# Kernel tuning notes

Hardware: AMD Instinct MI355X
Metric: run time of the kernel (lower is better)

The kernel has to match this reference:

```python
import jax, jax.numpy as jnp
import numpy as np

H = 2048          # hidden_size
NH = 16           # num query heads
NKV = 8           # num kv heads
HD = 128          # head_dim
T = 4096          # tokens (single causal prefill sequence)
THETA = 1000000.0
EPS = 1e-6
QS = NH * HD
KVS = NKV * HD
SCALE = HD ** -0.5


def setup_inputs() -> dict:
    key = jax.random.key(0)
    k0, k1, k2 = jax.random.split(key, 3)
    return {
        "positions": jnp.arange(T, dtype=jnp.int32),
        "hidden_states": jax.random.normal(k0, (T, H), jnp.float32),
        "w_qkv": jax.random.normal(k1, (H, QS + 2 * KVS), jnp.float32) * 0.02,
        "w_o": jax.random.normal(k2, (QS, H), jnp.float32) * 0.02,
        "q_norm_w": jnp.ones((HD,), jnp.float32),
        "k_norm_w": jnp.ones((HD,), jnp.float32),
    }


def _rmsnorm(x, w):
    # per-head RMSNorm over last dim (head_dim)
    return x * jax.lax.rsqrt(jnp.mean(x * x, axis=-1, keepdims=True) + EPS) * w


def _rope(x, cos, sin):
    # neox-style rotate-half RoPE; x: [T, nheads, HD], cos/sin: [T, 1, HD/2]
    x1, x2 = jnp.split(x, 2, axis=-1)
    return jnp.concatenate([x1 * cos - x2 * sin, x2 * cos + x1 * sin], axis=-1)


def reference(positions, hidden_states, w_qkv, w_o, q_norm_w, k_norm_w):
    # fused QKV projection then split
    qkv = hidden_states @ w_qkv                      # [T, QS+2*KVS]
    q, k, v = jnp.split(qkv, [QS, QS + KVS], axis=-1)
    q = _rmsnorm(q.reshape(T, NH, HD), q_norm_w)     # per-head QK RMSNorm
    k = _rmsnorm(k.reshape(T, NKV, HD), k_norm_w)
    v = v.reshape(T, NKV, HD)

    # RoPE over full head_dim
    inv_freq = 1.0 / (THETA ** (jnp.arange(0, HD, 2, dtype=jnp.float32) / HD))
    ang = positions.astype(jnp.float32)[:, None] * inv_freq  # [T, HD/2]
    cos = jnp.cos(ang)[:, None, :]
    sin = jnp.sin(ang)[:, None, :]
    q = _rope(q, cos, sin)
    k = _rope(k, cos, sin)

    # causal GQA attention (prefill path of RadixAttention)
    G = NH // NKV
    q4 = q.reshape(T, NKV, G, HD) * SCALE
    scores = jnp.einsum('tkgd,skd->kgts', q4, k)     # [NKV, G, T, T]
    causal = jnp.tril(jnp.ones((T, T), dtype=bool))
    scores = jnp.where(causal, scores, jnp.float32(-1e30))
    probs = jax.nn.softmax(scores, axis=-1)
    out = jnp.einsum('kgts,skd->tkgd', probs, v).reshape(T, QS)
    return out @ w_o
```

## Files before the change

### kernel.cpp

```cpp
#include <hip/hip_runtime.h>
#include <hip/hip_bf16.h>
#include <math.h>

#define T_TOK 4096
#define H_DIM 2048
#define NH 16
#define NKV 8
#define HD 128
#define QS (NH * HD)
#define KVS (NKV * HD)
#define QKV_W (QS + 2*KVS)
#define QSCALE (0.08838834764831845f * 1.4426950408889634f)
#define EPS 1e-6f

typedef short short8 __attribute__((ext_vector_type(8)));
typedef short short4v __attribute__((ext_vector_type(4)));
typedef float floatx4 __attribute__((ext_vector_type(4)));

#if __has_builtin(__builtin_amdgcn_exp2f)
#define EXP2(x) __builtin_amdgcn_exp2f(x)
#else
#define EXP2(x) exp2f(x)
#endif

__device__ __forceinline__ unsigned short f2bf(float f) {
    unsigned int u = __float_as_uint(f);
    unsigned int r = (u + 0x7FFFu + ((u >> 16) & 1u)) >> 16;
    return (unsigned short)r;
}
__device__ __forceinline__ float bf2f(unsigned short u) {
    unsigned int v = ((unsigned int)u) << 16;
    return __uint_as_float(v);
}
__device__ __forceinline__ unsigned int pk2(float a, float b) {
    union { __hip_bfloat162 h; unsigned int u; } c;
    c.h = __float22bfloat162_rn(make_float2(a, b));
    return c.u;
}

__device__ __forceinline__ void gload_lds16(const unsigned short* g, unsigned short* l) {
    __builtin_amdgcn_global_load_lds(
        (const __attribute__((address_space(1))) unsigned int*)(const void*)g,
        (__attribute__((address_space(3))) unsigned int*)(void*)l, 16, 0, 0);
}

__global__ __launch_bounds__(256) void cvt_bf16(const float* __restrict__ in,
                                                unsigned short* __restrict__ out) {
    int idx = (blockIdx.x * 256 + threadIdx.x) * 8;
    float4 v0 = *(const float4*)&in[idx];
    float4 v1 = *(const float4*)&in[idx + 4];
    short8 t;
    t[0] = (short)f2bf(v0.x); t[1] = (short)f2bf(v0.y);
    t[2] = (short)f2bf(v0.z); t[3] = (short)f2bf(v0.w);
    t[4] = (short)f2bf(v1.x); t[5] = (short)f2bf(v1.y);
    t[6] = (short)f2bf(v1.z); t[7] = (short)f2bf(v1.w);
    *(short8*)&out[idx] = t;
}

__global__ __launch_bounds__(256) void cvt_transpose(const float* __restrict__ in,
                                                     unsigned short* __restrict__ out,
                                                     int K, int N) {
    __shared__ __align__(16) unsigned short t[64][72];
    const int tid = threadIdx.x;
    const int n0 = blockIdx.x * 64, k0 = blockIdx.y * 64;
    const int r = tid >> 4, c4 = (tid & 15) * 4;
    #pragma unroll
    for (int i = 0; i < 4; ++i) {
        int kk = r + 16 * i;
        float4 v = *(const float4*)&in[(size_t)(k0 + kk) * N + n0 + c4];
        t[c4 + 0][kk] = f2bf(v.x); t[c4 + 1][kk] = f2bf(v.y);
        t[c4 + 2][kk] = f2bf(v.z); t[c4 + 3][kk] = f2bf(v.w);
    }
    __syncthreads();
    const int n = tid >> 2, c8 = (tid & 3) * 16;
    short8 a = *(const short8*)&t[n][c8];
    short8 b = *(const short8*)&t[n][c8 + 8];
    *(short8*)&out[(size_t)(n0 + n) * K + k0 + c8] = a;
    *(short8*)&out[(size_t)(n0 + n) * K + k0 + c8 + 8] = b;
}

template<bool C_BF16, int BN>
__global__ __launch_bounds__(512, 2) void gemm8p(const unsigned short* __restrict__ A, int lda,
                                                 const unsigned short* __restrict__ Bt, int ldb,
                                                 void* __restrict__ Cptr, int ldc, int K, int nbx) {
    constexpr int LDSTILE = 16384 + BN * 64;
    constexpr int NFRAG = BN / 64;
    __shared__ __align__(16) unsigned short lds[2 * LDSTILE];
    const int tid  = threadIdx.x;
    const int wave = tid >> 6, lane = tid & 63;
    const int quad = lane >> 4, l16 = lane & 15;
    const int wm = wave >> 2, wn = wave & 3;

    const int cpx = gridDim.x >> 3;
    const int swzb = (blockIdx.x & 7) * cpx + (blockIdx.x >> 3);
    const int by = swzb / nbx, bx = swzb % nbx;
    const int bm = by * 256, bn = bx * BN;

    const int ch0 = wave * 64 + lane, ch1 = 512 + ch0;
    const int r0 = ch0 >> 3, gc0 = ((ch0 & 7) ^ (r0 & 7)) * 8;
    const int r1 = ch1 >> 3, gc1 = ((ch1 & 7) ^ (r1 & 7)) * 8;
    const unsigned du0 = (unsigned)(wave * 64) * 8;
    const unsigned du1 = (unsigned)(512 + wave * 64) * 8;

    auto stageP = [&](const unsigned short* P, int bp, int ld,
                      unsigned short* dstbase, int rhalf, int kt) {
        unsigned short* dst = dstbase + rhalf * 64;
        gload_lds16(P + (size_t)(bp + rhalf + r0) * ld + kt * 64 + gc0, dst + du0);
        gload_lds16(P + (size_t)(bp + rhalf + r1) * ld + kt * 64 + gc1, dst + du1);
    };
    auto stage = [&](int kt, int buf) {
        unsigned short* ab = &lds[buf * LDSTILE];
        unsigned short* bb = ab + 16384;
        stageP(A, bm, lda, ab, 0, kt);
        stageP(A, bm, lda, ab, 128, kt);
        stageP(Bt, bn, ldb, bb, 0, kt);
        if (BN == 256) stageP(Bt, bn, ldb, bb, 128, kt);
    };

    floatx4 acc[8][NFRAG] = {};
    const int arowb = wm * 128 + l16;
    const int browb = wn * (BN / 4) + l16;
    const int sw = l16 & 7;

    auto compute = [&](int buf) {
        const unsigned short* ab = &lds[buf * LDSTILE];
        const unsigned short* bb = ab + 16384;
        __builtin_amdgcn_s_setprio(1);
        #pragma unroll
        for (int kk = 0; kk < 2; ++kk) {
            const int sl = ((kk * 4 + quad) ^ sw) * 8;
            short8 bfr[NFRAG];
            #pragma unroll
            for (int ni = 0; ni < NFRAG; ++ni)
                bfr[ni] = *(const short8*)&bb[(browb + ni * 16) * 64 + sl];
            #pragma unroll
            for (int mh = 0; mh < 2; ++mh) {
                short8 afr[4];
                #pragma unroll
                for (int mi = 0; mi < 4; ++mi)
                    afr[mi] = *(const short8*)&ab[(arowb + (mh * 4 + mi) * 16) * 64 + sl];
                #pragma unroll
                for (int mi = 0; mi < 4; ++mi)
                    #pragma unroll
                    for (int ni = 0; ni < NFRAG; ++ni)
                        acc[mh * 4 + mi][ni] =
                            __builtin_amdgcn_mfma_f32_16x16x32_bf16(afr[mi], bfr[ni], acc[mh * 4 + mi][ni], 0, 0, 0);
            }
        }
        __builtin_amdgcn_s_setprio(0);
    };

    const int NT = K >> 6;
    stage(0, 0);
    int cur = 0;
    for (int kt = 0; kt < NT; ++kt) {
        asm volatile("s_waitcnt vmcnt(0)" ::: "memory");
        __builtin_amdgcn_s_barrier();
        if (kt + 1 < NT) stage(kt + 1, cur ^ 1);
        compute(cur);
        cur ^= 1;
    }

    #pragma unroll
    for (int mi = 0; mi < 8; ++mi)
        #pragma unroll
        for (int ni = 0; ni < NFRAG; ++ni)
            #pragma unroll
            for (int r = 0; r < 4; ++r) {
                int row = bm + wm * 128 + mi * 16 + quad * 4 + r;
                int col = bn + wn * (BN / 4) + ni * 16 + l16;
                if (C_BF16)
                    ((unsigned short*)Cptr)[(size_t)row * ldc + col] = f2bf(acc[mi][ni][r]);
                else
                    ((float*)Cptr)[(size_t)row * ldc + col] = acc[mi][ni][r];
            }
}

__global__ __launch_bounds__(256) void rms_rope_bf16(unsigned short* __restrict__ qkv,
                                                     const int* __restrict__ positions,
                                                     const float* __restrict__ qw,
                                                     const float* __restrict__ kw) {
    const int t = blockIdx.x;
    const int wave = threadIdx.x >> 6;
    const int lane = threadIdx.x & 63;
    const float pos = (float)positions[t];
    unsigned short* row = qkv + (size_t)t * QKV_W;
    const float inv_freq = exp2f(-(float)lane * (19.931568569324174f / 64.0f));
    float sv, cv;
    sincosf(pos * inv_freq, &sv, &cv);
    for (int h = wave; h < NH + NKV; h += 4) {
        unsigned short* x = row + h * HD;
        const float* w = (h < NH) ? qw : kw;
        const float hs = (h < NH) ? QSCALE : 1.0f;
        float x1 = bf2f(x[lane]);
        float x2 = bf2f(x[lane + 64]);
        float ss = x1 * x1 + x2 * x2;
        #pragma unroll
        for (int off = 32; off > 0; off >>= 1) ss += __shfl_xor(ss, off, 64);
        float r = rsqrtf(ss * (1.0f / 128.0f) + EPS) * hs;
        float n1 = x1 * r * w[lane];
        float n2 = x2 * r * w[lane + 64];
        x[lane]      = f2bf(n1 * cv - n2 * sv);
        x[lane + 64] = f2bf(n2 * cv + n1 * sv);
    }
}

__global__ __launch_bounds__(256) void kv_pack(const unsigned short* __restrict__ qkv,
                                               unsigned short* __restrict__ Kp,
                                               unsigned short* __restrict__ Vp) {
    const int tile = blockIdx.x, kvh = blockIdx.y, tid = threadIdx.x;
    const int t0 = tile * 128;
    const size_t tb = (size_t)(kvh * 32 + tile) * 16384;
    #pragma unroll
    for (int i = 0; i < 8; ++i) {
        int cid = i * 256 + tid;
        int s = cid >> 4, c = cid & 15;
        short8 v = *(const short8*)&qkv[(size_t)(t0 + s) * QKV_W + QS + kvh * HD + c * 8];
        *(short8*)&Kp[tb + (s * 16 + (c ^ (s & 7))) * 8] = v;
    }
    __shared__ __align__(16) unsigned short Lt[128 * 136];
    #pragma unroll
    for (int i = 0; i < 8; ++i) {
        int cid = i * 256 + tid;
        int s = cid >> 4, c = cid & 15;
        short8 v = *(const short8*)&qkv[(size_t)(t0 + s) * QKV_W + QS + KVS + kvh * HD + c * 8];
        #pragma unroll
        for (int e = 0; e < 8; ++e) {
            int ee = (e + c) & 7;
            Lt[(c * 8 + ee) * 136 + s] = (unsigned short)v[ee];
        }
    }
    __syncthreads();
    #pragma unroll
    for (int i = 0; i < 8; ++i) {
        int cid = i * 256 + tid;
        int d = cid >> 4, cs = cid & 15;
        short8 v = *(const short8*)&Lt[d * 136 + cs * 8];
        short8 w;
        if ((d >> 3) & 1) {
            #pragma unroll
            for (int e = 0; e < 8; ++e) w[e] = v[e ^ 4];
        } else w = v;
        *(short8*)&Vp[tb + (d * 16 + (cs ^ (d & 7))) * 8] = w;
    }
}

__global__ __launch_bounds__(256, 2) void attn_mfma(unsigned short* __restrict__ qkv,
                                                    const unsigned short* __restrict__ Kp,
                                                    const unsigned short* __restrict__ Vp) {
    __shared__ __align__(16) unsigned short Ks[128 * 128];
    __shared__ __align__(16) unsigned short Vs[128 * 128];
    const int bx = blockIdx.x;
    const int h = bx & 15, kvh = h >> 1;
    const int g = bx >> 4;
    const int qt = (g < 16) ? (31 - g) : (g - 16);
    const int tid = threadIdx.x;
    const int wave = tid >> 6, lane = tid & 63;
    const int quad = lane >> 4, l16 = lane & 15;
    const int t0 = qt * 128;
    const int wrow0 = t0 + wave * 32;
    const int swz = l16 & 7;
    const int hsel = (l16 >> 3) & 1;
    const int vhalf = ((quad & 1) ^ hsel) * 4;
    const int q2 = quad >> 1;

    short8 qf[2][4];
    #pragma unroll
    for (int rt = 0; rt < 2; ++rt)
        #pragma unroll
        for (int ks = 0; ks < 4; ++ks) {
            int rowg = t0 + wave * 32 + rt * 16 + l16;
            qf[rt][ks] = *(const short8*)&qkv[(size_t)rowg * QKV_W + h * HD + ks * 32 + quad * 8];
        }

    float l_s[2] = {};
    floatx4 oacc[2][8] = {};

    for (int st = 0; st <= qt; ++st) {
        const int s0 = st * 128;
        const unsigned short* kb = Kp + (size_t)(kvh * 32 + st) * 16384;
        const unsigned short* vb = Vp + (size_t)(kvh * 32 + st) * 16384;
        #pragma unroll
        for (int i = 0; i < 8; ++i) {
            int ch = i * 256 + tid;
            gload_lds16(kb + (size_t)ch * 8, Ks + (i * 256 + wave * 64) * 8);
        }
        #pragma unroll
        for (int i = 0; i < 8; ++i) {
            int ch = i * 256 + tid;
            gload_lds16(vb + (size_t)ch * 8, Vs + (i * 256 + wave * 64) * 8);
        }
        __syncthreads();

        const bool diag = (st == qt);
        #pragma unroll
        for (int ct = 0; ct < 8; ++ct) {
            const int smin = s0 + ct * 16;
            if (diag && smin > wrow0 + 31) continue;
            floatx4 sacc[2] = {};
            #pragma unroll
            for (int ks = 0; ks < 4; ++ks) {
                short8 kfr = *(const short8*)&Ks[(ct * 16 + l16) * 128 + ((ks * 4 + quad) ^ swz) * 8];
                sacc[0] = __builtin_amdgcn_mfma_f32_16x16x32_bf16(kfr, qf[0][ks], sacc[0], 0, 0, 0);
                sacc[1] = __builtin_amdgcn_mfma_f32_16x16x32_bf16(kfr, qf[1][ks], sacc[1], 0, 0, 0);
            }
            short4v pp[2];
            #pragma unroll
            for (int rt = 0; rt < 2; ++rt) {
                const int tg = wrow0 + rt * 16 + l16;
                float p[4];
                float lsum = 0.0f;
                #pragma unroll
                for (int r = 0; r < 4; ++r) {
                    float s = sacc[rt][r];
                    if (diag && (smin + quad * 4 + r > tg)) s = -1e30f;
                    p[r] = EXP2(s);
                    lsum += p[r];
                }
                l_s[rt] += lsum;
                union { short4v s4; unsigned int u[2]; } pk;
                pk.u[0] = pk2(p[0], p[1]);
                pk.u[1] = pk2(p[2], p[3]);
                pp[rt] = pk.s4;
            }
            const int vc = (((ct * 2 + q2) ^ swz)) * 8 + vhalf;
#if __has_builtin(__builtin_amdgcn_mfma_f32_16x16x16bf16_1k)
            #pragma unroll
            for (int dct = 0; dct < 8; ++dct) {
                short4v bfr = *(const short4v*)&Vs[(dct * 16 + l16) * 128 + vc];
                oacc[0][dct] = __builtin_amdgcn_mfma_f32_16x16x16bf16_1k(pp[0], bfr, oacc[0][dct], 0, 0, 0);
                oacc[1][dct] = __builtin_amdgcn_mfma_f32_16x16x16bf16_1k(pp[1], bfr, oacc[1][dct], 0, 0, 0);
            }
#else
            #pragma unroll
            for (int dct = 0; dct < 8; ++dct) {
                union { short8 s8; short4v s4[2]; } b;
                b.s4[0] = *(const short4v*)&Vs[(dct * 16 + l16) * 128 + vc];
                b.s4[1] = short4v{0, 0, 0, 0};
                #pragma unroll
                for (int rt = 0; rt < 2; ++rt) {
                    union { short8 s8; short4v s4[2]; } a;
                    a.s4[0] = pp[rt];
                    a.s4[1] = short4v{0, 0, 0, 0};
                    oacc[rt][dct] = __builtin_amdgcn_mfma_f32_16x16x32_bf16(a.s8, b.s8, oacc[rt][dct], 0, 0, 0);
                }
            }
#endif
        }
        __syncthreads();
    }

    float lred[2];
    #pragma unroll
    for (int rt = 0; rt < 2; ++rt) {
        float l = l_s[rt];
        l += __shfl_xor(l, 16, 64);
        l += __shfl_xor(l, 32, 64);
        lred[rt] = l;
    }
    #pragma unroll
    for (int rt = 0; rt < 2; ++rt)
        #pragma unroll
        for (int r = 0; r < 4; ++r) {
            float l = __shfl(lred[rt], quad * 4 + r, 64);
            float linv = 1.0f / l;
            int rowg = t0 + wave * 32 + rt * 16 + quad * 4 + r;
            #pragma unroll
            for (int dct = 0; dct < 8; ++dct)
                qkv[(size_t)rowg * QKV_W + h * HD + dct * 16 + l16] = f2bf(oacc[rt][dct][r] * linv);
        }
}

extern "C" void kernel_launch(void* const* d_in, const int* in_sizes, int n_in,
                              void* d_out, int out_size, void* d_ws, size_t ws_size,
                              hipStream_t stream) {
    const int*   positions = (const int*)d_in[0];
    const float* hidden    = (const float*)d_in[1];
    const float* w_qkv     = (const float*)d_in[2];
    const float* w_o       = (const float*)d_in[3];
    const float* q_norm_w  = (const float*)d_in[4];
    const float* k_norm_w  = (const float*)d_in[5];
    float* out = (float*)d_out;

    unsigned short* qkvb   = (unsigned short*)d_ws;
    unsigned short* h_bf   = (unsigned short*)((char*)d_ws + ((size_t)32 << 20));
    unsigned short* Kp     = (unsigned short*)((char*)d_ws + ((size_t)32 << 20));
    unsigned short* Vp     = (unsigned short*)((char*)d_ws + ((size_t)40 << 20));
    unsigned short* wqkv_t = (unsigned short*)((char*)d_ws + ((size_t)48 << 20));
    unsigned short* wo_t   = (unsigned short*)((char*)d_ws + ((size_t)48 << 20));

    cvt_bf16<<<(T_TOK * H_DIM) / (256 * 8), 256, 0, stream>>>(hidden, h_bf);
    cvt_transpose<<<dim3(QKV_W / 64, H_DIM / 64), 256, 0, stream>>>(w_qkv, wqkv_t, H_DIM, QKV_W);
    gemm8p<true, 256><<<dim3(256), 512, 0, stream>>>(
        h_bf, H_DIM, wqkv_t, H_DIM, qkvb, QKV_W, H_DIM, QKV_W / 256);
    rms_rope_bf16<<<T_TOK, 256, 0, stream>>>(qkvb, positions, q_norm_w, k_norm_w);
    kv_pack<<<dim3(T_TOK / 128, NKV), 256, 0, stream>>>(qkvb, Kp, Vp);
    cvt_transpose<<<dim3(H_DIM / 64, QS / 64), 256, 0, stream>>>(w_o, wo_t, QS, H_DIM);
    attn_mfma<<<512, 256, 0, stream>>>(qkvb, Kp, Vp);
    gemm8p<false, 128><<<dim3(256), 512, 0, stream>>>(
        qkvb, QKV_W, wo_t, QS, out, H_DIM, QS, H_DIM / 128);
}
```

Baseline: 344.8 us.

## Switch attention MFMAs to 32x32x16 tiles with permlane32 swap for P

```diff
diff --git a/kernel.cpp b/kernel.cpp
--- a/kernel.cpp
+++ b/kernel.cpp
@@ -16,6 +16,8 @@
 typedef short short8 __attribute__((ext_vector_type(8)));
 typedef short short4v __attribute__((ext_vector_type(4)));
 typedef float floatx4 __attribute__((ext_vector_type(4)));
+typedef float floatx16 __attribute__((ext_vector_type(16)));
+typedef unsigned int uint2v __attribute__((ext_vector_type(2)));
 
 #if __has_builtin(__builtin_amdgcn_exp2f)
 #define EXP2(x) __builtin_amdgcn_exp2f(x)
@@ -236,12 +238,7 @@
         int cid = i * 256 + tid;
         int d = cid >> 4, cs = cid & 15;
         short8 v = *(const short8*)&Lt[d * 136 + cs * 8];
-        short8 w;
-        if ((d >> 3) & 1) {
-            #pragma unroll
-            for (int e = 0; e < 8; ++e) w[e] = v[e ^ 4];
-        } else w = v;
-        *(short8*)&Vp[tb + (d * 16 + (cs ^ (d & 7))) * 8] = w;
+        *(short8*)&Vp[tb + (d * 16 + (cs ^ (d & 7))) * 8] = v;
     }
 }
 
@@ -256,25 +253,19 @@
     const int qt = (g < 16) ? (31 - g) : (g - 16);
     const int tid = threadIdx.x;
     const int wave = tid >> 6, lane = tid & 63;
-    const int quad = lane >> 4, l16 = lane & 15;
+    const int t5 = lane & 31, hh = lane >> 5;
+    const int sw5 = t5 & 7;
     const int t0 = qt * 128;
     const int wrow0 = t0 + wave * 32;
-    const int swz = l16 & 7;
-    const int hsel = (l16 >> 3) & 1;
-    const int vhalf = ((quad & 1) ^ hsel) * 4;
-    const int q2 = quad >> 1;
-
-    short8 qf[2][4];
-    #pragma unroll
-    for (int rt = 0; rt < 2; ++rt)
-        #pragma unroll
-        for (int ks = 0; ks < 4; ++ks) {
-            int rowg = t0 + wave * 32 + rt * 16 + l16;
-            qf[rt][ks] = *(const short8*)&qkv[(size_t)rowg * QKV_W + h * HD + ks * 32 + quad * 8];
-        }
-
-    float l_s[2] = {};
-    floatx4 oacc[2][8] = {};
+    const int tg = wrow0 + t5;
+
+    short8 qf2[8];
+    #pragma unroll
+    for (int ks = 0; ks < 8; ++ks)
+        qf2[ks] = *(const short8*)&qkv[(size_t)tg * QKV_W + h * HD + ks * 16 + hh * 8];
+
+    float l_s = 0.0f;
+    floatx16 oacc[4] = {};
 
     for (int st = 0; st <= qt; ++st) {
         const int s0 = st * 128;
@@ -294,81 +285,70 @@
 
         const bool diag = (st == qt);
         #pragma unroll
-        for (int ct = 0; ct < 8; ++ct) {
-            const int smin = s0 + ct * 16;
+        for (int ct2 = 0; ct2 < 4; ++ct2) {
+            const int smin = s0 + ct2 * 32;
             if (diag && smin > wrow0 + 31) continue;
-            floatx4 sacc[2] = {};
-            #pragma unroll
-            for (int ks = 0; ks < 4; ++ks) {
-                short8 kfr = *(const short8*)&Ks[(ct * 16 + l16) * 128 + ((ks * 4 + quad) ^ swz) * 8];
-                sacc[0] = __builtin_amdgcn_mfma_f32_16x16x32_bf16(kfr, qf[0][ks], sacc[0], 0, 0, 0);
-                sacc[1] = __builtin_amdgcn_mfma_f32_16x16x32_bf16(kfr, qf[1][ks], sacc[1], 0, 0, 0);
-            }
-            short4v pp[2];
-            #pragma unroll
-            for (int rt = 0; rt < 2; ++rt) {
-                const int tg = wrow0 + rt * 16 + l16;
-                float p[4];
-                float lsum = 0.0f;
+            floatx16 sacc = {};
+            #pragma unroll
+            for (int ks = 0; ks < 8; ++ks) {
+                short8 kfr = *(const short8*)&Ks[((ct2 * 32 + t5) * 16 + ((2 * ks + hh) ^ sw5)) * 8];
+                sacc = __builtin_amdgcn_mfma_f32_32x32x16_bf16(kfr, qf2[ks], sacc, 0, 0, 0);
+            }
+            unsigned int w[8];
+            float lsum = 0.0f;
+            #pragma unroll
+            for (int i = 0; i < 8; ++i) {
+                const int r0i = 2 * i, r1i = 2 * i + 1;
+                const int sl0 = (r0i & 3) + 8 * (r0i >> 2) + 4 * hh;
+                float sa = sacc[r0i], sb = sacc[r1i];
+                if (diag && (smin + sl0 > tg))     sa = -1e30f;
+                if (diag && (smin + sl0 + 1 > tg)) sb = -1e30f;
+                float p0 = EXP2(sa), p1 = EXP2(sb);
+                lsum += p0 + p1;
+                w[i] = pk2(p0, p1);
+            }
+            l_s += lsum;
+            #pragma unroll
+            for (int m = 0; m < 2; ++m) {
+                union { short8 s8; unsigned int u[4]; } af;
+#if __has_builtin(__builtin_amdgcn_permlane32_swap)
+                uint2v x0 = __builtin_amdgcn_permlane32_swap(w[4 * m + 0], w[4 * m + 2], false, false);
+                uint2v x1 = __builtin_amdgcn_permlane32_swap(w[4 * m + 1], w[4 * m + 3], false, false);
+                af.u[0] = x0[0]; af.u[2] = x0[1];
+                af.u[1] = x1[0]; af.u[3] = x1[1];
+#else
+                unsigned p0 = (unsigned)__shfl_xor((int)w[4 * m + 0], 32, 64);
+                unsigned p1 = (unsigned)__shfl_xor((int)w[4 * m + 1], 32, 64);
+                unsigned p2 = (unsigned)__shfl_xor((int)w[4 * m + 2], 32, 64);
+                unsigned p3 = (unsigned)__shfl_xor((int)w[4 * m + 3], 32, 64);
+                af.u[0] = hh ? p2 : w[4 * m + 0];
+                af.u[1] = hh ? p3 : w[4 * m + 1];
+                af.u[2] = hh ? w[4 * m + 2] : p0;
+                af.u[3] = hh ? w[4 * m + 3] : p1;
+#endif
+                const int cs = ct2 * 4 + 2 * m + hh;
                 #pragma unroll
-                for (int r = 0; r < 4; ++r) {
-                    float s = sacc[rt][r];
-                    if (diag && (smin + quad * 4 + r > tg)) s = -1e30f;
-                    p[r] = EXP2(s);
-                    lsum += p[r];
+                for (int b = 0; b < 4; ++b) {
+                    const int d = b * 32 + t5;
+                    short8 vfr = *(const short8*)&Vs[(d * 16 + (cs ^ (d & 7))) * 8];
+                    oacc[b] = __builtin_amdgcn_mfma_f32_32x32x16_bf16(af.s8, vfr, oacc[b], 0, 0, 0);
                 }
-                l_s[rt] += lsum;
-                union { short4v s4; unsigned int u[2]; } pk;
-                pk.u[0] = pk2(p[0], p[1]);
-                pk.u[1] = pk2(p[2], p[3]);
-                pp[rt] = pk.s4;
-            }
-            const int vc = (((ct * 2 + q2) ^ swz)) * 8 + vhalf;
-#if __has_builtin(__builtin_amdgcn_mfma_f32_16x16x16bf16_1k)
-            #pragma unroll
-            for (int dct = 0; dct < 8; ++dct) {
-                short4v bfr = *(const short4v*)&Vs[(dct * 16 + l16) * 128 + vc];
-                oacc[0][dct] = __builtin_amdgcn_mfma_f32_16x16x16bf16_1k(pp[0], bfr, oacc[0][dct], 0, 0, 0);
-                oacc[1][dct] = __builtin_amdgcn_mfma_f32_16x16x16bf16_1k(pp[1], bfr, oacc[1][dct], 0, 0, 0);
-            }
-#else
-            #pragma unroll
-            for (int dct = 0; dct < 8; ++dct) {
-                union { short8 s8; short4v s4[2]; } b;
-                b.s4[0] = *(const short4v*)&Vs[(dct * 16 + l16) * 128 + vc];
-                b.s4[1] = short4v{0, 0, 0, 0};
-                #pragma unroll
-                for (int rt = 0; rt < 2; ++rt) {
-                    union { short8 s8; short4v s4[2]; } a;
-                    a.s4[0] = pp[rt];
-                    a.s4[1] = short4v{0, 0, 0, 0};
-                    oacc[rt][dct] = __builtin_amdgcn_mfma_f32_16x16x32_bf16(a.s8, b.s8, oacc[rt][dct], 0, 0, 0);
-                }
-            }
-#endif
+            }
         }
         __syncthreads();
     }
 
-    float lred[2];
-    #pragma unroll
-    for (int rt = 0; rt < 2; ++rt) {
-        float l = l_s[rt];
-        l += __shfl_xor(l, 16, 64);
-        l += __shfl_xor(l, 32, 64);
-        lred[rt] = l;
-    }
-    #pragma unroll
-    for (int rt = 0; rt < 2; ++rt)
-        #pragma unroll
-        for (int r = 0; r < 4; ++r) {
-            float l = __shfl(lred[rt], quad * 4 + r, 64);
-            float linv = 1.0f / l;
-            int rowg = t0 + wave * 32 + rt * 16 + quad * 4 + r;
-            #pragma unroll
-            for (int dct = 0; dct < 8; ++dct)
-                qkv[(size_t)rowg * QKV_W + h * HD + dct * 16 + l16] = f2bf(oacc[rt][dct][r] * linv);
-        }
+    float lred = l_s + __shfl_xor(l_s, 32, 64);
+    float linv = 1.0f / lred;
+    #pragma unroll
+    for (int r = 0; r < 16; ++r) {
+        const int tl = (r & 3) + 8 * (r >> 2) + 4 * hh;
+        float lv = __shfl(linv, tl, 64);
+        const int rowg = wrow0 + tl;
+        #pragma unroll
+        for (int b = 0; b < 4; ++b)
+            qkv[(size_t)rowg * QKV_W + h * HD + b * 32 + t5] = f2bf(oacc[b][r] * lv);
+    }
 }
 
 extern "C" void kernel_launch(void* const* d_in, const int* in_sizes, int n_in,
```

After: 361.9 us. 1.05x slower.
